# Kernel optimization log

Measured on AMD Instinct MI355X. Metric: run time of the kernel, lower is better.

## Reference

```python
import jax, jax.numpy as jnp
import numpy as np

B, T, C = 2, 2048, 2048
H = 16
D = C // H  # head_dim = 128
ROPE_BASE = 10000.0


def rope_cos_sin(seq_len, dim, dtype):
    inv_freq = 1.0 / (ROPE_BASE ** (jnp.arange(0, dim, 2, dtype=jnp.float32) / dim))
    t = jnp.arange(seq_len, dtype=jnp.float32)
    freqs = jnp.outer(t, inv_freq)              # [T, D/2]
    emb = jnp.concatenate([freqs, freqs], -1)   # [T, D]
    return emb.astype(dtype), None  # placeholder replaced below


def rotate_half(x):
    x1, x2 = jnp.split(x, 2, axis=-1)
    return jnp.concatenate([-x2, x1], axis=-1)


def setup_inputs() -> dict:
    key = jax.random.key(0)
    k1, k2, k3 = jax.random.split(key, 3)
    sc = 1.0 / np.sqrt(C)
    x = jax.random.normal(k1, (B, T, C), dtype=jnp.float32)
    w_qkv = jax.random.normal(k2, (C, 3 * C), dtype=jnp.float32) * sc
    w_out = jax.random.normal(k3, (C, C), dtype=jnp.float32) * sc
    return {"x": x, "w_qkv": w_qkv, "w_out": w_out}


def reference(x, w_qkv, w_out):
    Bq, Tq, Cq = x.shape
    qkv = x @ w_qkv                                    # [B,T,3C]
    q, k, v = jnp.split(qkv, 3, axis=-1)
    # [B,T,C] -> [B,H,T,D]
    q = q.reshape(Bq, Tq, H, D).transpose(0, 2, 1, 3)
    k = k.reshape(Bq, Tq, H, D).transpose(0, 2, 1, 3)
    v = v.reshape(Bq, Tq, H, D).transpose(0, 2, 1, 3)
    # RoPE
    inv_freq = 1.0 / (ROPE_BASE ** (jnp.arange(0, D, 2, dtype=jnp.float32) / D))
    freqs = jnp.outer(jnp.arange(Tq, dtype=jnp.float32), inv_freq)  # [T, D/2]
    emb = jnp.concatenate([freqs, freqs], -1)                        # [T, D]
    cos = jnp.cos(emb).astype(x.dtype)[None, None]                   # [1,1,T,D]
    sin = jnp.sin(emb).astype(x.dtype)[None, None]
    q = q * cos + rotate_half(q) * sin
    k = k * cos + rotate_half(k) * sin
    # causal SDPA
    scale = 1.0 / np.sqrt(D)
    att = jnp.einsum("bhqd,bhkd->bhqk", q, k) * scale
    causal = jnp.tril(jnp.ones((Tq, Tq), dtype=bool))
    att = jnp.where(causal[None, None], att, -jnp.inf)
    att = jax.nn.softmax(att, axis=-1)
    y = jnp.einsum("bhqk,bhkd->bhqd", att, v)          # [B,H,T,D]
    y = y.transpose(0, 2, 1, 3).reshape(Bq, Tq, Cq)
    return y @ w_out
```

## Files before the change

### kernel.cpp

```cpp
#include <hip/hip_runtime.h>
#include <hip/hip_bf16.h>
#include <type_traits>
#include <utility>

typedef unsigned short u16;
typedef unsigned int u32;

#define B_ 2
#define T_ 2048
#define C_ 2048
#define H_ 16
#define D_ 128
#define LDQKV 6144

typedef float float4v __attribute__((ext_vector_type(4)));
typedef short short8 __attribute__((ext_vector_type(8)));

__device__ inline u16 f2bf(float f) {
  u32 u = __builtin_bit_cast(u32, f);
  u32 r = u + 0x7fffu + ((u >> 16) & 1u);
  return (u16)(r >> 16);
}
__device__ inline float bfbits2f(u16 b) {
  return __builtin_bit_cast(float, (u32)b << 16);
}
__device__ inline u32 pack2bf(float a, float b) {
  u32 ua = (__builtin_bit_cast(u32, a) + 0x8000u) >> 16;
  u32 ub = (__builtin_bit_cast(u32, b) + 0x8000u) & 0xffff0000u;
  return ua | ub;
}

#if defined(__HIP_DEVICE_COMPILE__)
typedef __bf16 bf16x8 __attribute__((ext_vector_type(8)));

template <typename V, typename = void>
struct mfma_takes_short : std::false_type {};
template <typename V>
struct mfma_takes_short<V, std::void_t<decltype(__builtin_amdgcn_mfma_f32_16x16x32_bf16(
    std::declval<V>(), std::declval<V>(), std::declval<float4v>(), 0, 0, 0))>>
    : std::true_type {};

template <typename SV>
__device__ inline float4v mfma_bf16(SV a, SV b, float4v c) {
  if constexpr (mfma_takes_short<SV>::value) {
    return __builtin_amdgcn_mfma_f32_16x16x32_bf16(a, b, c, 0, 0, 0);
  } else {
    return __builtin_amdgcn_mfma_f32_16x16x32_bf16(
        __builtin_bit_cast(bf16x8, a), __builtin_bit_cast(bf16x8, b), c, 0, 0, 0);
  }
}

__device__ inline void async16(u16* lds, const u16* g) {
  typedef __attribute__((address_space(3))) void lds_void;
  typedef __attribute__((address_space(1))) const void g_void;
  __builtin_amdgcn_global_load_lds((g_void*)g, (lds_void*)lds, 16, 0, 0);
}
#endif

__global__ __launch_bounds__(256) void cast_f32_bf16(const float* __restrict__ s,
                                                     u16* __restrict__ d) {
  int i = (blockIdx.x * 256 + threadIdx.x) * 4;
  float4 v = *(const float4*)(s + i);
  alignas(8) u16 o[4] = {f2bf(v.x), f2bf(v.y), f2bf(v.z), f2bf(v.w)};
  *(uint2*)(d + i) = *(const uint2*)o;
}

__global__ __launch_bounds__(256) void castT_f32_bf16(const float* __restrict__ src,
                                                      u16* __restrict__ dst,
                                                      int R, int Cc) {
  __shared__ float tile[32][33];
  const int t = threadIdx.x;
  const int r0 = blockIdx.y * 32, c0 = blockIdx.x * 32;
  const int lr = t >> 3, lc = (t & 7) * 4;
  float4 v = *(const float4*)(src + (size_t)(r0 + lr) * Cc + c0 + lc);
  tile[lr][lc + 0] = v.x;
  tile[lr][lc + 1] = v.y;
  tile[lr][lc + 2] = v.z;
  tile[lr][lc + 3] = v.w;
  __syncthreads();
  alignas(8) u16 o[4];
#pragma unroll
  for (int j = 0; j < 4; ++j) o[j] = f2bf(tile[lc + j][lr]);
  *(uint2*)(dst + (size_t)(c0 + lr) * R + r0 + lc) = *(const uint2*)o;
}

__global__ __launch_bounds__(256) void vT_build(const u16* __restrict__ qkv,
                                                u16* __restrict__ Vt) {
  __shared__ u16 lt[64][72];
  const int tid = threadIdx.x;
  const int bh = blockIdx.x;
  const int tt = blockIdx.y;
  const int dd = blockIdx.z;
  const int b = bh >> 4, h = bh & 15;
  const int r = tid >> 2;
  const int c4 = (tid & 3) * 16;
  const u16* src = qkv + ((size_t)(b * T_ + tt * 64 + r)) * LDQKV + 2 * C_ + h * 128 + dd * 64 + c4;
  *(uint4*)&lt[r][c4] = *(const uint4*)src;
  *(uint4*)&lt[r][c4 + 8] = *(const uint4*)(src + 8);
  __syncthreads();
  alignas(16) u16 o[16];
#pragma unroll
  for (int j = 0; j < 16; ++j) o[j] = lt[c4 + j][r];
  u16* dst = Vt + ((size_t)(bh * 128 + dd * 64 + r)) * 2048 + tt * 64 + c4;
  *(uint4*)dst = *(const uint4*)o;
  *(uint4*)(dst + 8) = *(const uint4*)(o + 8);
}

template <bool CF32>
__global__ __launch_bounds__(512, 2) void gemm256_bt(const u16* __restrict__ A,
                                                     const u16* __restrict__ BT,
                                                     void* __restrict__ Cp,
                                                     int K, int lda, int ldbt, int ldc,
                                                     int nbx) {
#if defined(__HIP_DEVICE_COMPILE__)
  __shared__ alignas(16) u16 As[2][256 * 64];
  __shared__ alignas(16) u16 Bs[2][256 * 64];
  const int tid = threadIdx.x;
  const int lane = tid & 63;
  const int w = tid >> 6;
  const int wm = w >> 2, wn = w & 3;
  const int ml = lane & 15, qd = lane >> 4;
  const int nwg = gridDim.x;
  const int cpx = nwg >> 3;
  const int swz = (blockIdx.x & 7) * cpx + (blockIdx.x >> 3);
  const int by = swz / nbx, bx = swz - by * nbx;
  const int m0 = by * 256, n0 = bx * 256;
  const int rowoff = lane >> 3;
  const int chunk = ((lane & 7) ^ rowoff) * 8;
  int rA0[2], rA1[2], rB0[2], rB1[2];
#pragma unroll
  for (int j = 0; j < 2; ++j) {
    int g = w * 2 + j;
    rA0[j] = (g >> 3) * 128 + (g & 7) * 8;
    rA1[j] = (g >> 3) * 128 + 64 + (g & 7) * 8;
    rB0[j] = (g >> 2) * 64 + (g & 3) * 8;
    rB1[j] = (g >> 2) * 64 + 32 + (g & 3) * 8;
  }
  const int ntiles = K >> 6;
  const int niter = ntiles >> 1;

#define STG_A(bufi, h, kt)                                                       \
  do {                                                                           \
    async16(&As[bufi][rA##h[0] * 64],                                            \
            A + (size_t)(m0 + rA##h[0] + rowoff) * lda + (kt) * 64 + chunk);     \
    async16(&As[bufi][rA##h[1] * 64],                                            \
            A + (size_t)(m0 + rA##h[1] + rowoff) * lda + (kt) * 64 + chunk);     \
  } while (0)
#define STG_B(bufi, h, kt)                                                       \
  do {                                                                           \
    async16(&Bs[bufi][rB##h[0] * 64],                                            \
            BT + (size_t)(n0 + rB##h[0] + rowoff) * ldbt + (kt) * 64 + chunk);   \
    async16(&Bs[bufi][rB##h[1] * 64],                                            \
            BT + (size_t)(n0 + rB##h[1] + rowoff) * ldbt + (kt) * 64 + chunk);   \
  } while (0)
#define LDA8(bufi, mh)                                                           \
  do {                                                                           \
    _Pragma("unroll") for (int mt_ = 0; mt_ < 4; ++mt_)                          \
    _Pragma("unroll") for (int ks_ = 0; ks_ < 2; ++ks_)                          \
      a[mt_][ks_] = *(const short8*)&As[bufi][                                   \
          (wm * 128 + (mh) * 64 + mt_ * 16 + ml) * 64 +                          \
          (((qd + ks_ * 4) ^ (ml & 7)) * 8)];                                    \
  } while (0)
#define LDB4(bufi, nh)                                                           \
  do {                                                                           \
    _Pragma("unroll") for (int nt_ = 0; nt_ < 2; ++nt_)                          \
    _Pragma("unroll") for (int ks_ = 0; ks_ < 2; ++ks_)                          \
      b[nt_][ks_] = *(const short8*)&Bs[bufi][                                   \
          (wn * 64 + (nh) * 32 + nt_ * 16 + ml) * 64 +                           \
          (((qd + ks_ * 4) ^ (ml & 7)) * 8)];                                    \
  } while (0)
#define MMA16(mh, nh)                                                            \
  do {                                                                           \
    __builtin_amdgcn_s_setprio(1);                                               \
    _Pragma("unroll") for (int ks_ = 0; ks_ < 2; ++ks_)                          \
    _Pragma("unroll") for (int mt_ = 0; mt_ < 4; ++mt_)                          \
    _Pragma("unroll") for (int nt_ = 0; nt_ < 2; ++nt_)                          \
      acc[(mh) * 4 + mt_][(nh) * 2 + nt_] = mfma_bf16(                           \
          a[mt_][ks_], b[nt_][ks_], acc[(mh) * 4 + mt_][(nh) * 2 + nt_]);        \
    __builtin_amdgcn_s_setprio(0);                                               \
  } while (0)
#define BAR __builtin_amdgcn_s_barrier()
#define LGKM0 asm volatile("s_waitcnt lgkmcnt(0)" ::: "memory")
#define LGKM8 asm volatile("s_waitcnt lgkmcnt(8)" ::: "memory")
#define VM4 asm volatile("s_waitcnt vmcnt(4)" ::: "memory")

  float4v acc[8][4] = {};
  short8 a[4][2], b[2][2];

  STG_A(0, 0, 0);
  STG_B(0, 0, 0);
  STG_A(0, 1, 0);
  STG_B(0, 1, 0);
  STG_A(1, 0, 1);
  STG_B(1, 0, 1);
  VM4;
  BAR;

  for (int i = 0; i < niter; ++i) {
    const int tb = 2 * i + 1;
    const int t2 = (2 * i + 2 < ntiles) ? 2 * i + 2 : ntiles - 1;
    const int t3 = (2 * i + 3 < ntiles) ? 2 * i + 3 : ntiles - 1;
    LDA8(0, 0);
    LDB4(0, 0);
    STG_A(1, 1, tb);
    LGKM8;
    BAR; LGKM0; MMA16(0, 0); BAR;
    LDB4(0, 1);
    STG_B(1, 1, tb);
    BAR; LGKM0; MMA16(0, 1); BAR;
    LDA8(0, 1);
    LDB4(0, 0);
    STG_A(0, 0, t2);
    LGKM8;
    BAR; LGKM0; MMA16(1, 0); BAR;
    LDB4(0, 1);
    STG_B(0, 0, t2);
    VM4;
    BAR; LGKM0; MMA16(1, 1); BAR;
    LDA8(1, 0);
    LDB4(1, 0);
    STG_A(0, 1, t2);
    LGKM8;
    BAR; LGKM0; MMA16(0, 0); BAR;
    LDB4(1, 1);
    STG_B(0, 1, t2);
    BAR; LGKM0; MMA16(0, 1); BAR;
    LDA8(1, 1);
    LDB4(1, 0);
    STG_A(1, 0, t3);
    LGKM8;
    BAR; LGKM0; MMA16(1, 0); BAR;
    LDB4(1, 1);
    STG_B(1, 0, t3);
    VM4;
    BAR; LGKM0; MMA16(1, 1); BAR;
  }

#pragma unroll
  for (int mt = 0; mt < 8; ++mt) {
#pragma unroll
    for (int nt = 0; nt < 4; ++nt) {
#pragma unroll
      for (int r = 0; r < 4; ++r) {
        int row = m0 + wm * 128 + mt * 16 + qd * 4 + r;
        int col = n0 + wn * 64 + nt * 16 + ml;
        if constexpr (CF32) {
          ((float*)Cp)[(size_t)row * ldc + col] = acc[mt][nt][r];
        } else {
          ((u16*)Cp)[(size_t)row * ldc + col] = f2bf(acc[mt][nt][r]);
        }
      }
    }
  }
#undef STG_A
#undef STG_B
#undef LDA8
#undef LDB4
#undef MMA16
#undef BAR
#undef LGKM0
#undef LGKM8
#undef VM4
#endif
}

template <bool CF32>
__global__ __launch_bounds__(256) void gemm_bt(const u16* __restrict__ A,
                                               const u16* __restrict__ BT,
                                               void* __restrict__ Cp,
                                               int K, int lda, int ldbt, int ldc) {
#if defined(__HIP_DEVICE_COMPILE__)
  __shared__ u16 As[4096];
  __shared__ u16 Bs[4096];
  const int tid = threadIdx.x;
  const int lane = tid & 63;
  const int w = tid >> 6;
  const int wm = w & 1, wn = w >> 1;
  const int ml = lane & 15, qd = lane >> 4;
  const int m0 = blockIdx.y * 128, n0 = blockIdx.x * 128;
  const int sm = lane >> 2, sk = (lane & 3) * 8;
  const u16* gA[2];
  const u16* gB[2];
  u16 *lA[2], *lB[2];
#pragma unroll
  for (int r = 0; r < 2; ++r) {
    int seg = r * 4 + w;
    gA[r] = A + (size_t)(m0 + seg * 16 + sm) * lda + sk;
    gB[r] = BT + (size_t)(n0 + seg * 16 + sm) * ldbt + sk;
    lA[r] = As + seg * 512;
    lB[r] = Bs + seg * 512;
  }
  float4v acc[4][4] = {};
  for (int kk = 0; kk < K; kk += 32) {
    __syncthreads();
    async16(lA[0], gA[0] + kk);
    async16(lA[1], gA[1] + kk);
    async16(lB[0], gB[0] + kk);
    async16(lB[1], gB[1] + kk);
    __syncthreads();
    short8 a[4], b[4];
#pragma unroll
    for (int mt = 0; mt < 4; ++mt)
      a[mt] = *(const short8*)(As + (wm * 64 + mt * 16 + ml) * 32 + qd * 8);
#pragma unroll
    for (int nt = 0; nt < 4; ++nt)
      b[nt] = *(const short8*)(Bs + (wn * 64 + nt * 16 + ml) * 32 + qd * 8);
#pragma unroll
    for (int mt = 0; mt < 4; ++mt)
#pragma unroll
      for (int nt = 0; nt < 4; ++nt) acc[mt][nt] = mfma_bf16(a[mt], b[nt], acc[mt][nt]);
  }
#pragma unroll
  for (int mt = 0; mt < 4; ++mt) {
#pragma unroll
    for (int nt = 0; nt < 4; ++nt) {
#pragma unroll
      for (int r = 0; r < 4; ++r) {
        int row = m0 + wm * 64 + mt * 16 + qd * 4 + r;
        int col = n0 + wn * 64 + nt * 16 + ml;
        if constexpr (CF32) {
          ((float*)Cp)[(size_t)row * ldc + col] = acc[mt][nt][r];
        } else {
          ((u16*)Cp)[(size_t)row * ldc + col] = f2bf(acc[mt][nt][r]);
        }
      }
    }
  }
#endif
}

template <bool AF32, bool BF32, bool CF32>
__global__ __launch_bounds__(256) void gemm_mixed(const void* __restrict__ Ap,
                                                  const void* __restrict__ Bp,
                                                  void* __restrict__ Cp,
                                                  int M, int N, int K,
                                                  int lda, int ldb, int ldc) {
#if defined(__HIP_DEVICE_COMPILE__)
  __shared__ u16 As[64][40];
  __shared__ u16 Bs[64][40];
  const int tid = threadIdx.x;
  const int lane = tid & 63;
  const int w = tid >> 6;
  const int m0 = blockIdx.y * 64;
  const int n0 = blockIdx.x * 64;
  const int arow = tid >> 2, acol = (tid & 3) * 8;
  const int brow = tid >> 3, bcol = (tid & 7) * 8;
  const int ml = lane & 15, qd = lane >> 4;
  float4v acc[4] = {};
  for (int kk = 0; kk < K; kk += 32) {
    __syncthreads();
    if constexpr (AF32) {
      const float* A = (const float*)Ap;
      const float* src = A + (size_t)(m0 + arow) * lda + (kk + acol);
      float4 f0 = *(const float4*)src;
      float4 f1 = *(const float4*)(src + 4);
      alignas(16) u16 tmp[8] = {f2bf(f0.x), f2bf(f0.y), f2bf(f0.z), f2bf(f0.w),
                                f2bf(f1.x), f2bf(f1.y), f2bf(f1.z), f2bf(f1.w)};
      *(uint4*)(&As[arow][acol]) = *(const uint4*)tmp;
    } else {
      const u16* A = (const u16*)Ap;
      *(uint4*)(&As[arow][acol]) = *(const uint4*)(A + (size_t)(m0 + arow) * lda + (kk + acol));
    }
    if constexpr (BF32) {
      const float* Bm = (const float*)Bp;
      const float* src = Bm + (size_t)(kk + brow) * ldb + (n0 + bcol);
      float4 f0 = *(const float4*)src;
      float4 f1 = *(const float4*)(src + 4);
      float fv[8] = {f0.x, f0.y, f0.z, f0.w, f1.x, f1.y, f1.z, f1.w};
#pragma unroll
      for (int i = 0; i < 8; ++i) Bs[bcol + i][brow] = f2bf(fv[i]);
    } else {
      const u16* Bm = (const u16*)Bp;
      uint4 bv = *(const uint4*)(Bm + (size_t)(kk + brow) * ldb + (n0 + bcol));
      const u16* bsp = (const u16*)&bv;
#pragma unroll
      for (int i = 0; i < 8; ++i) Bs[bcol + i][brow] = bsp[i];
    }
    __syncthreads();
    short8 af = *(const short8*)(&As[w * 16 + ml][qd * 8]);
#pragma unroll
    for (int nt = 0; nt < 4; ++nt) {
      short8 bf = *(const short8*)(&Bs[nt * 16 + ml][qd * 8]);
      acc[nt] = mfma_bf16(af, bf, acc[nt]);
    }
  }
#pragma unroll
  for (int nt = 0; nt < 4; ++nt) {
#pragma unroll
    for (int r = 0; r < 4; ++r) {
      int row = m0 + w * 16 + qd * 4 + r;
      int col = n0 + nt * 16 + ml;
      if constexpr (CF32) {
        ((float*)Cp)[(size_t)row * ldc + col] = acc[nt][r];
      } else {
        ((u16*)Cp)[(size_t)row * ldc + col] = f2bf(acc[nt][r]);
      }
    }
  }
#endif
}

__global__ __launch_bounds__(256) void rope_inplace(u16* __restrict__ qkv, float qscale) {
  int idx = blockIdx.x * 256 + threadIdx.x;
  int d = idx & 63;
  int h = (idx >> 6) & 15;
  int t = (idx >> 10) & 2047;
  int b = idx >> 21;
  size_t row = (size_t)(b * T_ + t) * LDQKV;
  u16* qp = qkv + row + h * 128;
  u16* kp = qkv + row + C_ + h * 128;
  float q1 = bfbits2f(qp[d]);
  float q2 = bfbits2f(qp[d + 64]);
  float k1 = bfbits2f(kp[d]);
  float k2 = bfbits2f(kp[d + 64]);
  float invf = exp2f((float)d * -0.20762050593046012f);
  float fr = (float)t * invf;
  float sn, cs;
  sincosf(fr, &sn, &cs);
  qp[d] = f2bf((q1 * cs - q2 * sn) * qscale);
  qp[d + 64] = f2bf((q2 * cs + q1 * sn) * qscale);
  kp[d] = f2bf(k1 * cs - k2 * sn);
  kp[d + 64] = f2bf(k2 * cs + k1 * sn);
}

__global__ __launch_bounds__(256, 2) void attn_fwd2(u16* __restrict__ qkv,
                                                    const u16* __restrict__ Vt) {
#if defined(__HIP_DEVICE_COMPILE__)
  __shared__ alignas(16) u16 kS[64 * 128];
  __shared__ alignas(16) u16 vS[128 * 64];
  __shared__ alignas(16) u16 pS[4][32][72];
  const int tid = threadIdx.x;
  const int lane = tid & 63;
  const int w = tid >> 6;
  const int ml = lane & 15, qd = lane >> 4;
  const int gx = blockIdx.x;
  const int half = gx >> 8, rem = gx & 255;
  const int bh = rem >> 3, q3 = rem & 7;
  const int qt = half ? q3 : (15 - q3);
  const int b = bh >> 4, h = bh & 15;
  const int hc = h * 128;
  const int m0 = qt * 128;
  const size_t rb = (size_t)(b * T_);
  short8 qf[2][4];
#pragma unroll
  for (int m = 0; m < 2; ++m) {
    const u16* qp = qkv + (rb + m0 + w * 32 + m * 16 + ml) * LDQKV + hc;
#pragma unroll
    for (int k4 = 0; k4 < 4; ++k4) qf[m][k4] = *(const short8*)(qp + k4 * 32 + qd * 8);
  }
  float4v acc[2][8] = {};
  float mi[2] = {-1.0e30f, -1.0e30f}, li[2] = {0.f, 0.f};
  const int nchunk = 2 * qt + 2;
  const int krow0 = w * 16 + qd;
  const int vd0 = w * 32 + (lane >> 3);
  const int vsegoff = ((lane & 7) ^ (lane >> 3)) * 8;
  const size_t vtbase = ((size_t)bh * 128) * 2048;

  for (int c = 0; c < nchunk; ++c) {
    __syncthreads();
#pragma unroll
    for (int i = 0; i < 4; ++i) {
      int key = krow0 + i * 4;
      int seg = (ml ^ (i * 4 + qd)) * 8;
      async16(kS + (w * 4 + i) * 512,
              qkv + (rb + c * 64 + key) * LDQKV + C_ + hc + seg);
    }
#pragma unroll
    for (int i = 0; i < 4; ++i) {
      int d = vd0 + i * 8;
      async16(vS + (w * 4 + i) * 512,
              Vt + vtbase + (size_t)d * 2048 + c * 64 + vsegoff);
    }
    __syncthreads();
    if (c * 64 > m0 + w * 32 + 31) continue;
    float4v s[4][2] = {};
#pragma unroll
    for (int kt = 0; kt < 4; ++kt) {
#pragma unroll
      for (int k4 = 0; k4 < 4; ++k4) {
        int key = kt * 16 + ml;
        int slot = key * 16 + ((k4 * 4 + qd) ^ key);
        short8 kf = *(const short8*)(kS + ((kt * 16 + ml) * 16 + ((k4 * 4 + qd) ^ ml)) * 8);
        (void)key; (void)slot;
        s[kt][0] = mfma_bf16(kf, qf[0][k4], s[kt][0]);
        s[kt][1] = mfma_bf16(kf, qf[1][k4], s[kt][1]);
      }
    }
    const bool domask = (c * 64 + 63) > (m0 + w * 32);
    float alpha[2];
#pragma unroll
    for (int m = 0; m < 2; ++m) {
      int qrow = m0 + w * 32 + m * 16 + ml;
      if (domask) {
#pragma unroll
        for (int kt = 0; kt < 4; ++kt)
#pragma unroll
          for (int r = 0; r < 4; ++r) {
            int key = c * 64 + kt * 16 + qd * 4 + r;
            if (key > qrow) s[kt][m][r] = -1.0e30f;
          }
      }
      float mx = -1.0e30f;
#pragma unroll
      for (int kt = 0; kt < 4; ++kt)
#pragma unroll
        for (int r = 0; r < 4; ++r) mx = fmaxf(mx, s[kt][m][r]);
      mx = fmaxf(mx, __shfl_xor(mx, 16, 64));
      mx = fmaxf(mx, __shfl_xor(mx, 32, 64));
      float mnew = fmaxf(mi[m], mx);
      float a = __expf(mi[m] - mnew);
      float sm = 0.f;
#pragma unroll
      for (int kt = 0; kt < 4; ++kt)
#pragma unroll
        for (int r = 0; r < 4; ++r) {
          float p = __expf(s[kt][m][r] - mnew);
          s[kt][m][r] = p;
          sm += p;
        }
      sm += __shfl_xor(sm, 16, 64);
      sm += __shfl_xor(sm, 32, 64);
      li[m] = li[m] * a + sm;
      mi[m] = mnew;
      alpha[m] = a;
#pragma unroll
      for (int kt = 0; kt < 4; ++kt) {
        uint2 pk;
        pk.x = pack2bf(s[kt][m][0], s[kt][m][1]);
        pk.y = pack2bf(s[kt][m][2], s[kt][m][3]);
        *(uint2*)&pS[w][m * 16 + ml][kt * 16 + qd * 4] = pk;
      }
    }
#pragma unroll
    for (int m = 0; m < 2; ++m) {
#pragma unroll
      for (int r = 0; r < 4; ++r) {
        float aq = __shfl(alpha[m], qd * 4 + r, 64);
#pragma unroll
        for (int dt = 0; dt < 8; ++dt) acc[m][dt][r] *= aq;
      }
    }
#pragma unroll
    for (int k2 = 0; k2 < 2; ++k2) {
      short8 pa0 = *(const short8*)&pS[w][ml][k2 * 32 + qd * 8];
      short8 pa1 = *(const short8*)&pS[w][16 + ml][k2 * 32 + qd * 8];
#pragma unroll
      for (int dt = 0; dt < 8; ++dt) {
        int d = dt * 16 + ml;
        short8 vf = *(const short8*)(vS + (d * 8 + ((k2 * 4 + qd) ^ (ml & 7))) * 8);
        acc[0][dt] = mfma_bf16(pa0, vf, acc[0][dt]);
        acc[1][dt] = mfma_bf16(pa1, vf, acc[1][dt]);
      }
    }
  }
#pragma unroll
  for (int m = 0; m < 2; ++m) {
#pragma unroll
    for (int r = 0; r < 4; ++r) {
      float inv = 1.0f / __shfl(li[m], qd * 4 + r, 64);
      size_t row = rb + m0 + w * 32 + m * 16 + qd * 4 + r;
#pragma unroll
      for (int dt = 0; dt < 8; ++dt)
        qkv[row * LDQKV + hc + dt * 16 + ml] = f2bf(acc[m][dt][r] * inv);
    }
  }
#endif
}

__global__ __launch_bounds__(256, 2) void attn_fwd(u16* __restrict__ qkv) {
#if defined(__HIP_DEVICE_COMPILE__)
  __shared__ alignas(16) u16 ks[64][136];
  __shared__ alignas(16) u16 vt[128][72];
  __shared__ alignas(16) u16 pb[4][32][72];
  const int tid = threadIdx.x;
  const int lane = tid & 63;
  const int w = tid >> 6;
  const int ml = lane & 15, qd = lane >> 4;
  const int gx = blockIdx.x;
  const int half = gx >> 8;
  const int rem = gx & 255;
  const int bh = rem >> 3;
  const int q3 = rem & 7;
  const int qt = half ? q3 : (15 - q3);
  const int b = bh >> 4, h = bh & 15;
  const int hc = h * 128;
  const int m0 = qt * 128;
  const size_t rb = (size_t)(b * T_);
  short8 qf[2][4];
#pragma unroll
  for (int m = 0; m < 2; ++m) {
    const u16* qp = qkv + (rb + m0 + w * 32 + m * 16 + ml) * LDQKV + hc;
#pragma unroll
    for (int k4 = 0; k4 < 4; ++k4) qf[m][k4] = *(const short8*)(qp + k4 * 32 + qd * 8);
  }
  float4v acc[2][8] = {};
  float mi[2][4], li[2][4];
#pragma unroll
  for (int m = 0; m < 2; ++m)
#pragma unroll
    for (int r = 0; r < 4; ++r) { mi[m][r] = -1.0e30f; li[m][r] = 0.f; }
  const float scale = 0.08838834764831845f;
  const int srow = tid >> 2;
  const int scol = (tid & 3) * 32;
  const int nchunk = 2 * qt + 2;
  for (int c = 0; c < nchunk; ++c) {
    __syncthreads();
    {
      const u16* kp = qkv + (rb + c * 64 + srow) * LDQKV + C_ + hc + scol;
      const u16* vp = qkv + (rb + c * 64 + srow) * LDQKV + 2 * C_ + hc + scol;
#pragma unroll
      for (int i = 0; i < 4; ++i)
        *(uint4*)&ks[srow][scol + i * 8] = *(const uint4*)(kp + i * 8);
#pragma unroll
      for (int i = 0; i < 4; ++i) {
        uint4 vv = *(const uint4*)(vp + i * 8);
        const u16* e = (const u16*)&vv;
#pragma unroll
        for (int t = 0; t < 8; ++t) vt[scol + i * 8 + t][srow] = e[t];
      }
    }
    __syncthreads();
    if (c * 64 > m0 + w * 32 + 31) continue;
    float4v s[2][4] = {};
#pragma unroll
    for (int t = 0; t < 4; ++t) {
#pragma unroll
      for (int k4 = 0; k4 < 4; ++k4) {
        short8 bf = *(const short8*)(&ks[t * 16 + ml][k4 * 32 + qd * 8]);
        s[0][t] = mfma_bf16(qf[0][k4], bf, s[0][t]);
        s[1][t] = mfma_bf16(qf[1][k4], bf, s[1][t]);
      }
    }
    const bool domask = (c * 64 + 63) > (m0 + w * 32);
#pragma unroll
    for (int m = 0; m < 2; ++m) {
      float al[4];
#pragma unroll
      for (int r = 0; r < 4; ++r) {
        float x0 = s[m][0][r] * scale;
        float x1 = s[m][1][r] * scale;
        float x2 = s[m][2][r] * scale;
        float x3 = s[m][3][r] * scale;
        if (domask) {
          int row = m0 + w * 32 + m * 16 + qd * 4 + r;
          int j0 = c * 64 + ml;
          if (j0 > row) x0 = -1.0e30f;
          if (j0 + 16 > row) x1 = -1.0e30f;
          if (j0 + 32 > row) x2 = -1.0e30f;
          if (j0 + 48 > row) x3 = -1.0e30f;
        }
        float mx = fmaxf(fmaxf(x0, x1), fmaxf(x2, x3));
        mx = fmaxf(mx, __shfl_xor(mx, 1));
        mx = fmaxf(mx, __shfl_xor(mx, 2));
        mx = fmaxf(mx, __shfl_xor(mx, 4));
        mx = fmaxf(mx, __shfl_xor(mx, 8));
        float mnew = fmaxf(mi[m][r], mx);
        float a = __expf(mi[m][r] - mnew);
        float p0 = __expf(x0 - mnew);
        float p1 = __expf(x1 - mnew);
        float p2 = __expf(x2 - mnew);
        float p3 = __expf(x3 - mnew);
        float sm = p0 + p1 + p2 + p3;
        sm += __shfl_xor(sm, 1);
        sm += __shfl_xor(sm, 2);
        sm += __shfl_xor(sm, 4);
        sm += __shfl_xor(sm, 8);
        li[m][r] = li[m][r] * a + sm;
        mi[m][r] = mnew;
        al[r] = a;
        int prow = m * 16 + qd * 4 + r;
        pb[w][prow][ml] = f2bf(p0);
        pb[w][prow][16 + ml] = f2bf(p1);
        pb[w][prow][32 + ml] = f2bf(p2);
        pb[w][prow][48 + ml] = f2bf(p3);
      }
#pragma unroll
      for (int d = 0; d < 8; ++d) {
        acc[m][d][0] *= al[0];
        acc[m][d][1] *= al[1];
        acc[m][d][2] *= al[2];
        acc[m][d][3] *= al[3];
      }
    }
#pragma unroll
    for (int k2 = 0; k2 < 2; ++k2) {
      short8 pa0 = *(const short8*)(&pb[w][ml][k2 * 32 + qd * 8]);
      short8 pa1 = *(const short8*)(&pb[w][16 + ml][k2 * 32 + qd * 8]);
#pragma unroll
      for (int d = 0; d < 8; ++d) {
        short8 vf = *(const short8*)(&vt[d * 16 + ml][k2 * 32 + qd * 8]);
        acc[0][d] = mfma_bf16(pa0, vf, acc[0][d]);
        acc[1][d] = mfma_bf16(pa1, vf, acc[1][d]);
      }
    }
  }
#pragma unroll
  for (int m = 0; m < 2; ++m) {
#pragma unroll
    for (int r = 0; r < 4; ++r) {
      float inv = 1.0f / li[m][r];
      size_t row = rb + m0 + w * 32 + m * 16 + qd * 4 + r;
#pragma unroll
      for (int d = 0; d < 8; ++d)
        qkv[row * LDQKV + hc + d * 16 + ml] = f2bf(acc[m][d][r] * inv);
    }
  }
#endif
}

extern "C" void kernel_launch(void* const* d_in, const int* in_sizes, int n_in,
                              void* d_out, int out_size, void* d_ws, size_t ws_size,
                              hipStream_t stream) {
  const float* x = (const float*)d_in[0];
  const float* wqkv = (const float*)d_in[1];
  const float* wout = (const float*)d_in[2];
  float* out = (float*)d_out;
  char* ws = (char*)d_ws;
  u16* qkv = (u16*)ws;

  const size_t MB = 1024 * 1024;
  if (ws_size >= 96 * MB) {
    u16* xb = (u16*)(ws + 48 * MB);
    u16* wqkvT = (u16*)(ws + 64 * MB);
    u16* Vt = (u16*)(ws + 64 * MB);
    u16* woutT = (u16*)(ws + 88 * MB);
    cast_f32_bf16<<<dim3(8192), dim3(256), 0, stream>>>(x, xb);
    castT_f32_bf16<<<dim3(192, 64), dim3(256), 0, stream>>>(wqkv, wqkvT, 2048, 6144);
    castT_f32_bf16<<<dim3(64, 64), dim3(256), 0, stream>>>(wout, woutT, 2048, 2048);
    gemm256_bt<false><<<dim3(384), dim3(512), 0, stream>>>(
        xb, wqkvT, qkv, 2048, 2048, 2048, 6144, 24);
    rope_inplace<<<dim3(16384), dim3(256), 0, stream>>>(qkv, 0.08838834764831845f);
    vT_build<<<dim3(32, 32, 2), dim3(256), 0, stream>>>(qkv, Vt);
    attn_fwd2<<<dim3(512), dim3(256), 0, stream>>>(qkv, Vt);
    gemm_bt<true><<<dim3(16, 32), dim3(256), 0, stream>>>(
        qkv, woutT, out, 2048, 6144, 2048, 2048);
  } else {
    gemm_mixed<true, true, false><<<dim3(96, 64), dim3(256), 0, stream>>>(
        x, wqkv, qkv, 4096, 6144, 2048, 2048, 6144, 6144);
    rope_inplace<<<dim3(16384), dim3(256), 0, stream>>>(qkv, 1.0f);
    attn_fwd<<<dim3(512), dim3(256), 0, stream>>>(qkv);
    gemm_mixed<false, true, true><<<dim3(32, 64), dim3(256), 0, stream>>>(
        qkv, wout, out, 4096, 2048, 2048, 6144, 2048, 2048);
  }
}
```

Before: 428.3 us.

## Keep both B fragment halves in registers and deepen GEMM prefetch schedule

The 256x256 GEMM main loop now holds both halves of the B fragment in registers, so the second pair of MMA quadrants no longer reloads B from LDS. The global-to-LDS staging is reordered: the prologue prefetches all four quarter-tiles of the second buffer, stores are issued earlier, and the vmcnt wait is relaxed to 8, allowing more loads in flight. This trims LDS traffic and some waits at the cost of more VGPRs for the B fragments, which may affect occupancy or spilling. Unused variables are also removed from the attention QK loop.

```diff
diff --git a/kernel.cpp b/kernel.cpp
--- a/kernel.cpp
+++ b/kernel.cpp
@@ -165,7 +165,7 @@
   do {                                                                           \
     _Pragma("unroll") for (int nt_ = 0; nt_ < 2; ++nt_)                          \
     _Pragma("unroll") for (int ks_ = 0; ks_ < 2; ++ks_)                          \
-      b[nt_][ks_] = *(const short8*)&Bs[bufi][                                   \
+      b[nh][nt_][ks_] = *(const short8*)&Bs[bufi][                               \
           (wn * 64 + (nh) * 32 + nt_ * 16 + ml) * 64 +                           \
           (((qd + ks_ * 4) ^ (ml & 7)) * 8)];                                    \
   } while (0)
@@ -176,16 +176,17 @@
     _Pragma("unroll") for (int mt_ = 0; mt_ < 4; ++mt_)                          \
     _Pragma("unroll") for (int nt_ = 0; nt_ < 2; ++nt_)                          \
       acc[(mh) * 4 + mt_][(nh) * 2 + nt_] = mfma_bf16(                           \
-          a[mt_][ks_], b[nt_][ks_], acc[(mh) * 4 + mt_][(nh) * 2 + nt_]);        \
+          a[mt_][ks_], b[nh][nt_][ks_], acc[(mh) * 4 + mt_][(nh) * 2 + nt_]);    \
     __builtin_amdgcn_s_setprio(0);                                               \
   } while (0)
 #define BAR __builtin_amdgcn_s_barrier()
 #define LGKM0 asm volatile("s_waitcnt lgkmcnt(0)" ::: "memory")
 #define LGKM8 asm volatile("s_waitcnt lgkmcnt(8)" ::: "memory")
-#define VM4 asm volatile("s_waitcnt vmcnt(4)" ::: "memory")
+#define VM8 asm volatile("s_waitcnt vmcnt(8)" ::: "memory")
 
   float4v acc[8][4] = {};
-  short8 a[4][2], b[2][2];
+  short8 a[4][2];
+  short8 b[2][2][2];
 
   STG_A(0, 0, 0);
   STG_B(0, 0, 0);
@@ -193,47 +194,42 @@
   STG_B(0, 1, 0);
   STG_A(1, 0, 1);
   STG_B(1, 0, 1);
-  VM4;
+  STG_A(1, 1, 1);
+  STG_B(1, 1, 1);
+  VM8;
   BAR;
 
   for (int i = 0; i < niter; ++i) {
-    const int tb = 2 * i + 1;
     const int t2 = (2 * i + 2 < ntiles) ? 2 * i + 2 : ntiles - 1;
     const int t3 = (2 * i + 3 < ntiles) ? 2 * i + 3 : ntiles - 1;
     LDA8(0, 0);
     LDB4(0, 0);
-    STG_A(1, 1, tb);
     LGKM8;
     BAR; LGKM0; MMA16(0, 0); BAR;
     LDB4(0, 1);
-    STG_B(1, 1, tb);
+    STG_A(0, 0, t2);
+    STG_B(0, 0, t2);
     BAR; LGKM0; MMA16(0, 1); BAR;
     LDA8(0, 1);
-    LDB4(0, 0);
-    STG_A(0, 0, t2);
-    LGKM8;
+    STG_B(0, 1, t2);
     BAR; LGKM0; MMA16(1, 0); BAR;
-    LDB4(0, 1);
-    STG_B(0, 0, t2);
-    VM4;
-    BAR; LGKM0; MMA16(1, 1); BAR;
+    STG_A(0, 1, t2);
+    VM8;
+    BAR; MMA16(1, 1); BAR;
     LDA8(1, 0);
     LDB4(1, 0);
-    STG_A(0, 1, t2);
     LGKM8;
     BAR; LGKM0; MMA16(0, 0); BAR;
     LDB4(1, 1);
-    STG_B(0, 1, t2);
+    STG_A(1, 0, t3);
+    STG_B(1, 0, t3);
     BAR; LGKM0; MMA16(0, 1); BAR;
     LDA8(1, 1);
-    LDB4(1, 0);
-    STG_A(1, 0, t3);
-    LGKM8;
+    STG_B(1, 1, t3);
     BAR; LGKM0; MMA16(1, 0); BAR;
-    LDB4(1, 1);
-    STG_B(1, 0, t3);
-    VM4;
-    BAR; LGKM0; MMA16(1, 1); BAR;
+    STG_A(1, 1, t3);
+    VM8;
+    BAR; MMA16(1, 1); BAR;
   }
 
 #pragma unroll
@@ -260,7 +256,7 @@
 #undef BAR
 #undef LGKM0
 #undef LGKM8
-#undef VM4
+#undef VM8
 #endif
 }
 
@@ -478,10 +474,7 @@
     for (int kt = 0; kt < 4; ++kt) {
 #pragma unroll
       for (int k4 = 0; k4 < 4; ++k4) {
-        int key = kt * 16 + ml;
-        int slot = key * 16 + ((k4 * 4 + qd) ^ key);
         short8 kf = *(const short8*)(kS + ((kt * 16 + ml) * 16 + ((k4 * 4 + qd) ^ ml)) * 8);
-        (void)key; (void)slot;
         s[kt][0] = mfma_bf16(kf, qf[0][k4], s[kt][0]);
         s[kt][1] = mfma_bf16(kf, qf[1][k4], s[kt][1]);
       }
```

Measured after the change: 441.1 us. +3.0%, slower.

## Double-buffer K/V tiles in attention kernel and shrink P staging buffer

Applied to the files above, without the earlier changes.

The attention kernel now keeps two LDS buffers for K and V and issues the async load of the next chunk before computing the current one. The goal is to hide global-memory latency behind the MFMA and softmax work, and to cut the two barriers per chunk down to one wait plus a barrier. The P staging buffer is halved: it is written and consumed in two 32-key halves per chunk. This roughly doubles K/V shared memory (about 64KB total), which may reduce how many blocks fit per CU relative to the launch bound of 2.

```diff
diff --git a/kernel.cpp b/kernel.cpp
--- a/kernel.cpp
+++ b/kernel.cpp
@@ -426,9 +426,9 @@
 __global__ __launch_bounds__(256, 2) void attn_fwd2(u16* __restrict__ qkv,
                                                     const u16* __restrict__ Vt) {
 #if defined(__HIP_DEVICE_COMPILE__)
-  __shared__ alignas(16) u16 kS[64 * 128];
-  __shared__ alignas(16) u16 vS[128 * 64];
-  __shared__ alignas(16) u16 pS[4][32][72];
+  __shared__ alignas(16) u16 kS[2][64 * 128];
+  __shared__ alignas(16) u16 vS[2][128 * 64];
+  __shared__ alignas(16) u16 pS[4][32][40];
   const int tid = threadIdx.x;
   const int lane = tid & 63;
   const int w = tid >> 6;
@@ -456,103 +456,116 @@
   const int vsegoff = ((lane & 7) ^ (lane >> 3)) * 8;
   const size_t vtbase = ((size_t)bh * 128) * 2048;
 
+#define STAGE(cc, bi)                                                        \
+  do {                                                                       \
+    _Pragma("unroll") for (int i_ = 0; i_ < 4; ++i_) {                       \
+      int key_ = krow0 + i_ * 4;                                             \
+      int seg_ = (ml ^ (i_ * 4 + qd)) * 8;                                   \
+      async16(kS[bi] + (w * 4 + i_) * 512,                                   \
+              qkv + (rb + (cc) * 64 + key_) * LDQKV + C_ + hc + seg_);       \
+    }                                                                        \
+    _Pragma("unroll") for (int i_ = 0; i_ < 4; ++i_) {                       \
+      int d_ = vd0 + i_ * 8;                                                 \
+      async16(vS[bi] + (w * 4 + i_) * 512,                                   \
+              Vt + vtbase + (size_t)d_ * 2048 + (cc) * 64 + vsegoff);        \
+    }                                                                        \
+  } while (0)
+
+  STAGE(0, 0);
+  asm volatile("s_waitcnt vmcnt(0)" ::: "memory");
+  __syncthreads();
+
   for (int c = 0; c < nchunk; ++c) {
+    const int cur = c & 1;
+    if (c + 1 < nchunk) STAGE(c + 1, cur ^ 1);
+    if (c * 64 <= m0 + w * 32 + 31) {
+      const u16* kb = kS[cur];
+      const u16* vb = vS[cur];
+      float4v s[4][2] = {};
+#pragma unroll
+      for (int kt = 0; kt < 4; ++kt) {
+#pragma unroll
+        for (int k4 = 0; k4 < 4; ++k4) {
+          short8 kf = *(const short8*)(kb + ((kt * 16 + ml) * 16 + ((k4 * 4 + qd) ^ ml)) * 8);
+          s[kt][0] = mfma_bf16(kf, qf[0][k4], s[kt][0]);
+          s[kt][1] = mfma_bf16(kf, qf[1][k4], s[kt][1]);
+        }
+      }
+      const bool domask = (c * 64 + 63) > (m0 + w * 32);
+      float alpha[2];
+#pragma unroll
+      for (int m = 0; m < 2; ++m) {
+        int qrow = m0 + w * 32 + m * 16 + ml;
+        if (domask) {
+#pragma unroll
+          for (int kt = 0; kt < 4; ++kt)
+#pragma unroll
+            for (int r = 0; r < 4; ++r) {
+              int key = c * 64 + kt * 16 + qd * 4 + r;
+              if (key > qrow) s[kt][m][r] = -1.0e30f;
+            }
+        }
+        float mx = -1.0e30f;
+#pragma unroll
+        for (int kt = 0; kt < 4; ++kt)
+#pragma unroll
+          for (int r = 0; r < 4; ++r) mx = fmaxf(mx, s[kt][m][r]);
+        mx = fmaxf(mx, __shfl_xor(mx, 16, 64));
+        mx = fmaxf(mx, __shfl_xor(mx, 32, 64));
+        float mnew = fmaxf(mi[m], mx);
+        float a = __expf(mi[m] - mnew);
+        float sm = 0.f;
+#pragma unroll
+        for (int kt = 0; kt < 4; ++kt)
+#pragma unroll
+          for (int r = 0; r < 4; ++r) {
+            float p = __expf(s[kt][m][r] - mnew);
+            s[kt][m][r] = p;
+            sm += p;
+          }
+        sm += __shfl_xor(sm, 16, 64);
+        sm += __shfl_xor(sm, 32, 64);
+        li[m] = li[m] * a + sm;
+        mi[m] = mnew;
+        alpha[m] = a;
+      }
+#pragma unroll
+      for (int m = 0; m < 2; ++m) {
+#pragma unroll
+        for (int r = 0; r < 4; ++r) {
+          float aq = __shfl(alpha[m], qd * 4 + r, 64);
+#pragma unroll
+          for (int dt = 0; dt < 8; ++dt) acc[m][dt][r] *= aq;
+        }
+      }
+#pragma unroll
+      for (int k2 = 0; k2 < 2; ++k2) {
+#pragma unroll
+        for (int m = 0; m < 2; ++m) {
+#pragma unroll
+          for (int ktl = 0; ktl < 2; ++ktl) {
+            int kt = k2 * 2 + ktl;
+            uint2 pk;
+            pk.x = pack2bf(s[kt][m][0], s[kt][m][1]);
+            pk.y = pack2bf(s[kt][m][2], s[kt][m][3]);
+            *(uint2*)&pS[w][m * 16 + ml][ktl * 16 + qd * 4] = pk;
+          }
+        }
+        short8 pa0 = *(const short8*)&pS[w][ml][qd * 8];
+        short8 pa1 = *(const short8*)&pS[w][16 + ml][qd * 8];
+#pragma unroll
+        for (int dt = 0; dt < 8; ++dt) {
+          int d = dt * 16 + ml;
+          short8 vf = *(const short8*)(vb + (d * 8 + ((k2 * 4 + qd) ^ (ml & 7))) * 8);
+          acc[0][dt] = mfma_bf16(pa0, vf, acc[0][dt]);
+          acc[1][dt] = mfma_bf16(pa1, vf, acc[1][dt]);
+        }
+      }
+    }
+    asm volatile("s_waitcnt vmcnt(0)" ::: "memory");
     __syncthreads();
-#pragma unroll
-    for (int i = 0; i < 4; ++i) {
-      int key = krow0 + i * 4;
-      int seg = (ml ^ (i * 4 + qd)) * 8;
-      async16(kS + (w * 4 + i) * 512,
-              qkv + (rb + c * 64 + key) * LDQKV + C_ + hc + seg);
-    }
-#pragma unroll
-    for (int i = 0; i < 4; ++i) {
-      int d = vd0 + i * 8;
-      async16(vS + (w * 4 + i) * 512,
-              Vt + vtbase + (size_t)d * 2048 + c * 64 + vsegoff);
-    }
-    __syncthreads();
-    if (c * 64 > m0 + w * 32 + 31) continue;
-    float4v s[4][2] = {};
-#pragma unroll
-    for (int kt = 0; kt < 4; ++kt) {
-#pragma unroll
-      for (int k4 = 0; k4 < 4; ++k4) {
-        int key = kt * 16 + ml;
-        int slot = key * 16 + ((k4 * 4 + qd) ^ key);
-        short8 kf = *(const short8*)(kS + ((kt * 16 + ml) * 16 + ((k4 * 4 + qd) ^ ml)) * 8);
-        (void)key; (void)slot;
-        s[kt][0] = mfma_bf16(kf, qf[0][k4], s[kt][0]);
-        s[kt][1] = mfma_bf16(kf, qf[1][k4], s[kt][1]);
-      }
-    }
-    const bool domask = (c * 64 + 63) > (m0 + w * 32);
-    float alpha[2];
-#pragma unroll
-    for (int m = 0; m < 2; ++m) {
-      int qrow = m0 + w * 32 + m * 16 + ml;
-      if (domask) {
-#pragma unroll
-        for (int kt = 0; kt < 4; ++kt)
-#pragma unroll
-          for (int r = 0; r < 4; ++r) {
-            int key = c * 64 + kt * 16 + qd * 4 + r;
-            if (key > qrow) s[kt][m][r] = -1.0e30f;
-          }
-      }
-      float mx = -1.0e30f;
-#pragma unroll
-      for (int kt = 0; kt < 4; ++kt)
-#pragma unroll
-        for (int r = 0; r < 4; ++r) mx = fmaxf(mx, s[kt][m][r]);
-      mx = fmaxf(mx, __shfl_xor(mx, 16, 64));
-      mx = fmaxf(mx, __shfl_xor(mx, 32, 64));
-      float mnew = fmaxf(mi[m], mx);
-      float a = __expf(mi[m] - mnew);
-      float sm = 0.f;
-#pragma unroll
-      for (int kt = 0; kt < 4; ++kt)
-#pragma unroll
-        for (int r = 0; r < 4; ++r) {
-          float p = __expf(s[kt][m][r] - mnew);
-          s[kt][m][r] = p;
-          sm += p;
-        }
-      sm += __shfl_xor(sm, 16, 64);
-      sm += __shfl_xor(sm, 32, 64);
-      li[m] = li[m] * a + sm;
-      mi[m] = mnew;
-      alpha[m] = a;
-#pragma unroll
-      for (int kt = 0; kt < 4; ++kt) {
-        uint2 pk;
-        pk.x = pack2bf(s[kt][m][0], s[kt][m][1]);
-        pk.y = pack2bf(s[kt][m][2], s[kt][m][3]);
-        *(uint2*)&pS[w][m * 16 + ml][kt * 16 + qd * 4] = pk;
-      }
-    }
-#pragma unroll
-    for (int m = 0; m < 2; ++m) {
-#pragma unroll
-      for (int r = 0; r < 4; ++r) {
-        float aq = __shfl(alpha[m], qd * 4 + r, 64);
-#pragma unroll
-        for (int dt = 0; dt < 8; ++dt) acc[m][dt][r] *= aq;
-      }
-    }
-#pragma unroll
-    for (int k2 = 0; k2 < 2; ++k2) {
-      short8 pa0 = *(const short8*)&pS[w][ml][k2 * 32 + qd * 8];
-      short8 pa1 = *(const short8*)&pS[w][16 + ml][k2 * 32 + qd * 8];
-#pragma unroll
-      for (int dt = 0; dt < 8; ++dt) {
-        int d = dt * 16 + ml;
-        short8 vf = *(const short8*)(vS + (d * 8 + ((k2 * 4 + qd) ^ (ml & 7))) * 8);
-        acc[0][dt] = mfma_bf16(pa0, vf, acc[0][dt]);
-        acc[1][dt] = mfma_bf16(pa1, vf, acc[1][dt]);
-      }
-    }
-  }
+  }
+#undef STAGE
 #pragma unroll
   for (int m = 0; m < 2; ++m) {
 #pragma unroll
```

Measured after the change: 426.5 us. About the same (-0.4%).
